# Kernel tuning notes

Measured on AMD Instinct MI355X. Metric: run time of the kernel, lower is better.

## Reference

```python
import jax, jax.numpy as jnp
import numpy as np

NEG_INF = -1.0e9
LN_EPS = 1e-5
LEAK = 0.2


def setup_inputs() -> dict:
    key = jax.random.key(0)
    ks = jax.random.split(key, 8)
    B, C, T, N, H = 8, 64, 24, 512, 2
    hd = C // H
    x = jax.random.normal(ks[0], (B, C, T, N), dtype=jnp.float32)
    gso = jax.random.randint(ks[1], (N, N), 0, 2, dtype=jnp.int32)
    # torch nn.Linear weights are (out, in); xavier-ish scale
    s = (2.0 / (C + C)) ** 0.5
    Wq = jax.random.normal(ks[2], (C, C), dtype=jnp.float32) * s
    Wk = jax.random.normal(ks[3], (C, C), dtype=jnp.float32) * s
    Wv = jax.random.normal(ks[4], (C, C), dtype=jnp.float32) * s
    sa = (2.0 / (H + hd)) ** 0.5
    a_src = jax.random.normal(ks[5], (H, hd), dtype=jnp.float32) * sa
    a_dst = jax.random.normal(ks[6], (H, hd), dtype=jnp.float32) * sa
    ln_gamma = jnp.ones((C,), dtype=jnp.float32)
    ln_beta = jnp.zeros((C,), dtype=jnp.float32)
    return {"x": x, "gso": gso, "Wq": Wq, "Wk": Wk, "Wv": Wv,
            "a_src": a_src, "a_dst": a_dst, "ln_gamma": ln_gamma, "ln_beta": ln_beta}


def _spatial_gat(x, gso, Wq, Wk, Wv, a_src, a_dst, ln_gamma, ln_beta):
    B, C, T, N = x.shape
    H, hd = a_src.shape
    # (B, C, T, N) -> (B*T, N, C)
    xr = jnp.transpose(x, (0, 2, 3, 1)).reshape(B * T, N, C)
    # torch Linear: y = x @ W.T
    Q = jnp.einsum('bnc,dc->bnd', xr, Wq).reshape(B * T, N, H, hd)
    K = jnp.einsum('bnc,dc->bnd', xr, Wk).reshape(B * T, N, H, hd)
    V = jnp.einsum('bnc,dc->bnd', xr, Wv).reshape(B * T, N, H, hd)
    # additive GAT scores, all heads at once
    s_src = jnp.einsum('bnhd,hd->bnh', Q, a_src)  # (BT, N, H)
    s_dst = jnp.einsum('bnhd,hd->bnh', K, a_dst)  # (BT, N, H)
    scores = jax.nn.leaky_relu(s_src[:, :, None, :] + s_dst[:, None, :, :], LEAK)  # (BT, Ni, Nj, H)
    mask = jnp.where(gso == 0, jnp.float32(NEG_INF), jnp.float32(0.0))  # (N, N)
    scores = scores + mask[None, :, :, None]
    attn = jax.nn.softmax(scores, axis=2)  # softmax over destination j
    out = jnp.einsum('bijh,bjhd->bihd', attn, V)  # (BT, N, H, hd)
    out = out.reshape(B * T, N, C)
    # LayerNorm over channel dim
    mu = jnp.mean(out, axis=-1, keepdims=True)
    var = jnp.var(out, axis=-1, keepdims=True)
    out = (out - mu) * jax.lax.rsqrt(var + LN_EPS) * ln_gamma + ln_beta
    # back to (B, C, T, N)
    return jnp.transpose(out.reshape(B, T, N, C), (0, 3, 1, 2))


def reference(x, gso, Wq, Wk, Wv, a_src, a_dst, ln_gamma, ln_beta):
    return _spatial_gat(x, gso, Wq, Wk, Wv, a_src, a_dst, ln_gamma, ln_beta)
```

## Files before the change

### kernel.cpp

```cpp
#include <hip/hip_runtime.h>

#define CDIM 64
#define TDIM 24
#define NDIM 512
#define NBT  192

typedef float    float4v __attribute__((ext_vector_type(4)));
typedef _Float16 half8v  __attribute__((ext_vector_type(8)));
typedef _Float16 half2v  __attribute__((ext_vector_type(2)));


__global__ void k0_maskbits(const int* __restrict__ gso, unsigned* __restrict__ bits) {
  int tg = blockIdx.x * 256 + threadIdx.x;
  int i  = tg >> 4;
  int ks = tg & 15;
  const int* row = gso + i * NDIM + ks * 32;
  unsigned w = 0;
#pragma unroll
  for (int b = 0; b < 32; ++b) w |= (row[b] != 0 ? (1u << b) : 0u);
  bits[ks * NDIM + i] = w;
}

struct SmemK1 {
  union {
    _Float16 xt[256][72];
    _Float16 vt[64][264];
  } big;
  _Float16 wv[64][72];
  _Float16 wext[16][72];
};

__launch_bounds__(256, 2)
__global__ void k1_qkv(const float* __restrict__ x,  const float* __restrict__ Wq,
                       const float* __restrict__ Wk, const float* __restrict__ Wv,
                       const float* __restrict__ a_src, const float* __restrict__ a_dst,
                       _Float16* __restrict__ VT_g,
                       float* __restrict__ s_src_g, float* __restrict__ s_dst_g) {
  __shared__ SmemK1 sm;
  const int t    = threadIdx.x;
  const int half = blockIdx.x;
  const int bt   = blockIdx.y;
  const int b    = bt / TDIM, tt = bt % TDIM;
  const int n0   = half * 256;

  for (int it = 0; it < 16; ++it) {
    int idx = it * 256 + t;
    int d = idx >> 6, k = idx & 63;
    sm.wv[d][k] = (_Float16)Wv[idx];
  }
  for (int it = 0; it < 32; ++it) {
    int idx = it * 256 + t;
    int cp  = idx >> 8;
    int n   = idx & 255;
    int c0  = cp * 2;
    const float* base = x + ((size_t)(b * CDIM + c0) * TDIM + tt) * NDIM + n0 + n;
    float v0 = base[0];
    float v1 = base[(size_t)TDIM * NDIM];
    half2v p; p[0] = (_Float16)v0; p[1] = (_Float16)v1;
    *(half2v*)&sm.big.xt[n][c0] = p;
  }
  for (int z = 4 * 72 + t; z < 16 * 72; z += 256) ((_Float16*)sm.wext)[z] = (_Float16)0.0f;
  if (t < 64) {
    int c = t;
    float s0 = 0.f, s1 = 0.f, d0 = 0.f, d1 = 0.f;
    for (int d = 0; d < 32; ++d) {
      s0 += a_src[d]      * Wq[d * 64 + c];
      s1 += a_src[32 + d] * Wq[(32 + d) * 64 + c];
      d0 += a_dst[d]      * Wk[d * 64 + c];
      d1 += a_dst[32 + d] * Wk[(32 + d) * 64 + c];
    }
    sm.wext[0][c] = (_Float16)s0; sm.wext[1][c] = (_Float16)s1;
    sm.wext[2][c] = (_Float16)d0; sm.wext[3][c] = (_Float16)d1;
  }
  __syncthreads();

  const int lane = t & 63, w = t >> 6;
  const int m = lane & 15, quad = lane >> 4;
  const int mbase = w * 64;

  float4v acc[4][5];
#pragma unroll
  for (int mt = 0; mt < 4; ++mt)
#pragma unroll
    for (int nt = 0; nt < 5; ++nt)
#pragma unroll
      for (int r = 0; r < 4; ++r) acc[mt][nt][r] = 0.f;

#pragma unroll
  for (int ks = 0; ks < 2; ++ks) {
    half8v af[4], bf[5];
#pragma unroll
    for (int mt = 0; mt < 4; ++mt)
      af[mt] = *(const half8v*)&sm.big.xt[mbase + mt * 16 + m][ks * 32 + quad * 8];
#pragma unroll
    for (int nt = 0; nt < 4; ++nt)
      bf[nt] = *(const half8v*)&sm.wv[nt * 16 + m][ks * 32 + quad * 8];
    bf[4] = *(const half8v*)&sm.wext[m][ks * 32 + quad * 8];
#pragma unroll
    for (int mt = 0; mt < 4; ++mt)
#pragma unroll
      for (int nt = 0; nt < 5; ++nt)
        acc[mt][nt] = __builtin_amdgcn_mfma_f32_16x16x32_f16(af[mt], bf[nt], acc[mt][nt], 0, 0, 0);
  }

  if (m < 4) {
    float* base = (m < 2 ? s_src_g : s_dst_g) + (size_t)(bt * 2 + (m & 1)) * NDIM;
#pragma unroll
    for (int mt = 0; mt < 4; ++mt)
#pragma unroll
      for (int r = 0; r < 4; ++r)
        base[n0 + mbase + mt * 16 + quad * 4 + r] = acc[mt][4][r];
  }
  __syncthreads();

#pragma unroll
  for (int mt = 0; mt < 4; ++mt)
#pragma unroll
    for (int nt = 0; nt < 4; ++nt)
#pragma unroll
      for (int r = 0; r < 4; ++r) {
        int node = mbase + mt * 16 + quad * 4 + r;
        int c    = nt * 16 + m;
        sm.big.vt[c][node] = (_Float16)acc[mt][nt][r];
      }
  __syncthreads();

  const unsigned* vts = (const unsigned*)sm.big.vt;
  unsigned* outdw = (unsigned*)VT_g;
  for (int it = 0; it < 32; ++it) {
    int idx = it * 256 + t;
    int c = idx >> 7, jd = idx & 127;
    outdw[(size_t)(bt * 64 + c) * 256 + half * 128 + jd] = vts[c * 132 + jd];
  }
}

struct SmemK2 {
  union {
    _Float16 vt[64][256];
    float otile[64][65];
  } big;
  union {
    float sdst[2][512];
    struct { float rsum[4][64]; float rsq[4][64]; float mu[64]; float rs[64]; } ln;
  } u2;
  float ssrc[2][64];
  unsigned maskT[16][64];
};

__launch_bounds__(256, 3)
__global__ void k2_attn(const _Float16* __restrict__ VT_g,
                        const float* __restrict__ s_src_g, const float* __restrict__ s_dst_g,
                        const unsigned* __restrict__ bits,
                        const float* __restrict__ gamma, const float* __restrict__ beta,
                        float* __restrict__ out) {
  __shared__ SmemK2 sm;
  const int t     = threadIdx.x;
  const int itile = blockIdx.x;
  const int bt    = blockIdx.y;
  const int i0    = itile * 64;
  const int b     = bt / TDIM, tt = bt % TDIM;

  for (int it = 0; it < 4; ++it) {
    int idx = it * 256 + t;
    ((float*)sm.u2.sdst)[idx] = s_dst_g[(size_t)bt * 2 * NDIM + idx];
  }
  if (t < 128) {
    int h = t >> 6, i = t & 63;
    sm.ssrc[h][i] = s_src_g[(size_t)(bt * 2 + h) * NDIM + i0 + i];
  }
  for (int it = 0; it < 4; ++it) {
    int idx = it * 256 + t;
    int ks = idx >> 6, i = idx & 63;
    sm.maskT[ks][i] = bits[ks * NDIM + i0 + i];
  }

  const int lane = t & 63, w = t >> 6;
  const int h = w >> 1, ihalf = w & 1;
  const int m = lane & 15, quad = lane >> 4;

  float4v acc[2][2];
#pragma unroll
  for (int mt = 0; mt < 2; ++mt)
#pragma unroll
    for (int nt = 0; nt < 2; ++nt)
#pragma unroll
      for (int r = 0; r < 4; ++r) acc[mt][nt][r] = 0.f;
  float ssum[2] = {0.f, 0.f};

  __syncthreads();
  float ss[2];
  ss[0] = sm.ssrc[h][ihalf * 32 + m];
  ss[1] = sm.ssrc[h][ihalf * 32 + 16 + m];

  for (int jh = 0; jh < 2; ++jh) {
    if (jh) __syncthreads();
    const unsigned* src_dw = (const unsigned*)VT_g + (size_t)bt * 64 * 256 + jh * 128;
    unsigned* vdw = (unsigned*)sm.big.vt;
    for (int it = 0; it < 32; ++it) {
      int idx = it * 256 + t;
      int c = idx >> 7, jd = idx & 127;
      vdw[c * 128 + (jd ^ ((c & 7) * 4))] = src_dw[(size_t)c * 256 + jd];
    }
    __syncthreads();

#pragma unroll
    for (int ksl = 0; ksl < 8; ++ksl) {
      int ks = jh * 8 + ksl;
      const float* dj = &sm.u2.sdst[h][ks * 32 + quad * 8];
      float djv[8];
#pragma unroll
      for (int q = 0; q < 8; ++q) djv[q] = dj[q];

      half8v af[2];
#pragma unroll
      for (int mt = 0; mt < 2; ++mt) {
        unsigned word = sm.maskT[ks][ihalf * 32 + mt * 16 + m];
        unsigned byte = (word >> (quad * 8)) & 0xffu;
        float s = ss[mt];
        half8v a;
        float lsum = 0.f;
#pragma unroll
        for (int jj = 0; jj < 8; ++jj) {
          float xv = s + djv[jj];
          xv = fmaxf(xv, 0.2f * xv);
          float e = ((byte >> jj) & 1u) ? __expf(xv - 4.f) : 0.f;
          _Float16 e16 = (_Float16)e;
          a[jj] = e16;
          lsum += (float)e16;
        }
        ssum[mt] += lsum;
        af[mt] = a;
      }
      int jo = ksl * 32 + quad * 8;
      int c0 = h * 32 + m, c1 = h * 32 + 16 + m;
      half8v b0 = *(const half8v*)&sm.big.vt[c0][jo ^ ((c0 & 7) * 8)];
      half8v b1 = *(const half8v*)&sm.big.vt[c1][jo ^ ((c1 & 7) * 8)];
      acc[0][0] = __builtin_amdgcn_mfma_f32_16x16x32_f16(af[0], b0, acc[0][0], 0, 0, 0);
      acc[0][1] = __builtin_amdgcn_mfma_f32_16x16x32_f16(af[0], b1, acc[0][1], 0, 0, 0);
      acc[1][0] = __builtin_amdgcn_mfma_f32_16x16x32_f16(af[1], b0, acc[1][0], 0, 0, 0);
      acc[1][1] = __builtin_amdgcn_mfma_f32_16x16x32_f16(af[1], b1, acc[1][1], 0, 0, 0);
    }
  }

#pragma unroll
  for (int mt = 0; mt < 2; ++mt) {
    ssum[mt] += __shfl_xor(ssum[mt], 16);
    ssum[mt] += __shfl_xor(ssum[mt], 32);
  }
  float inv[2] = {1.f / ssum[0], 1.f / ssum[1]};

  __syncthreads();
#pragma unroll
  for (int mt = 0; mt < 2; ++mt)
#pragma unroll
    for (int r = 0; r < 4; ++r) {
      float sv = __shfl(inv[mt], quad * 4 + r);
      int i_loc = ihalf * 32 + mt * 16 + quad * 4 + r;
#pragma unroll
      for (int nt = 0; nt < 2; ++nt) {
        int c = h * 32 + nt * 16 + m;
        sm.big.otile[i_loc][c] = acc[mt][nt][r] * sv;
      }
    }
  __syncthreads();

  {
    int i = t & 63, cg = t >> 6;
    float s1 = 0.f, s2 = 0.f;
#pragma unroll
    for (int cc = 0; cc < 16; ++cc) {
      float v = sm.big.otile[i][cg * 16 + cc];
      s1 += v; s2 += v * v;
    }
    sm.u2.ln.rsum[cg][i] = s1;
    sm.u2.ln.rsq[cg][i]  = s2;
  }
  __syncthreads();
  if (t < 64) {
    int i = t;
    float s1 = 0.f, s2 = 0.f;
#pragma unroll
    for (int cg = 0; cg < 4; ++cg) { s1 += sm.u2.ln.rsum[cg][i]; s2 += sm.u2.ln.rsq[cg][i]; }
    float mu  = s1 * (1.f / 64.f);
    float var = s2 * (1.f / 64.f) - mu * mu;
    sm.u2.ln.mu[i] = mu;
    sm.u2.ln.rs[i] = rsqrtf(var + 1e-5f);
  }
  __syncthreads();
  {
    int i = t & 63, cg = t >> 6;
    float mu = sm.u2.ln.mu[i], rs = sm.u2.ln.rs[i];
    int n = i0 + i;
#pragma unroll
    for (int cc = 0; cc < 16; ++cc) {
      int c = cg * 16 + cc;
      float v = (sm.big.otile[i][c] - mu) * rs * gamma[c] + beta[c];
      out[((size_t)(b * CDIM + c) * TDIM + tt) * NDIM + n] = v;
    }
  }
}

extern "C" void kernel_launch(void* const* d_in, const int* in_sizes, int n_in,
                              void* d_out, int out_size, void* d_ws, size_t ws_size,
                              hipStream_t stream) {
  const float* x     = (const float*)d_in[0];
  const int*   gso   = (const int*)d_in[1];
  const float* Wq    = (const float*)d_in[2];
  const float* Wk    = (const float*)d_in[3];
  const float* Wv    = (const float*)d_in[4];
  const float* a_src = (const float*)d_in[5];
  const float* a_dst = (const float*)d_in[6];
  const float* gamma = (const float*)d_in[7];
  const float* beta  = (const float*)d_in[8];
  float* out = (float*)d_out;

  char* ws = (char*)d_ws;
  _Float16* VT_g   = (_Float16*)ws;
  float*    s_src  = (float*)(ws + 12582912);
  float*    s_dst  = (float*)(ws + 13369344);
  unsigned* bits   = (unsigned*)(ws + 14155776);

  k0_maskbits<<<32, 256, 0, stream>>>(gso, bits);
  k1_qkv<<<dim3(2, NBT), 256, 0, stream>>>(x, Wq, Wk, Wv, a_src, a_dst, VT_g, s_src, s_dst);
  k2_attn<<<dim3(8, NBT), 256, 0, stream>>>(VT_g, s_src, s_dst, bits, gamma, beta, out);
}
```

Before: 145.9 us.

## Restructure mask to byte mask, compute softmax denominator via MFMA, shrink tiles

Mask bits become a byte mask (0x00/0xFF per half lane). In the attention kernel the mask is applied with a perm-and-AND on packed fp16 instead of per-element branches. The row-sum of exponentials is now computed by an extra MFMA against a ones vector, which replaces the scalar accumulation and shuffles. Leaky-relu is folded into a max of two FMAs. The folded a_src/a_dst weight projection moves into the prep kernel, and the QKV kernel uses 128-node tiles for higher occupancy. V tiles are streamed in four chunks with vectorised 16-byte loads. The cost is an extra MFMA per tile and smaller tiles in k2, which means more barriers.

After: 130.4 us. 10.6% less time.

```diff
diff --git a/kernel.cpp b/kernel.cpp
--- a/kernel.cpp
+++ b/kernel.cpp
@@ -10,77 +10,77 @@
 typedef _Float16 half2v  __attribute__((ext_vector_type(2)));
 
 
-__global__ void k0_maskbits(const int* __restrict__ gso, unsigned* __restrict__ bits) {
-  int tg = blockIdx.x * 256 + threadIdx.x;
-  int i  = tg >> 4;
-  int ks = tg & 15;
-  const int* row = gso + i * NDIM + ks * 32;
-  unsigned w = 0;
-#pragma unroll
-  for (int b = 0; b < 32; ++b) w |= (row[b] != 0 ? (1u << b) : 0u);
-  bits[ks * NDIM + i] = w;
+__global__ void k0_prep(const int* __restrict__ gso,
+                        const float* __restrict__ Wq, const float* __restrict__ Wk,
+                        const float* __restrict__ a_src, const float* __restrict__ a_dst,
+                        unsigned* __restrict__ maskb, float* __restrict__ wfold) {
+  int t = threadIdx.x;
+  if (blockIdx.x < 256) {
+    int tg = blockIdx.x * 256 + t;
+    int4 g = ((const int4*)gso)[tg];
+    unsigned w = (g.x ? 0x000000FFu : 0u) | (g.y ? 0x0000FF00u : 0u) |
+                 (g.z ? 0x00FF0000u : 0u) | (g.w ? 0xFF000000u : 0u);
+    maskb[tg] = w;
+  } else {
+    int r = t >> 6, c = t & 63;
+    const float* av = (r & 2) ? a_dst : a_src;
+    const float* W  = (r & 2) ? Wk : Wq;
+    int off = (r & 1) * 32;
+    float s = 0.f;
+#pragma unroll
+    for (int d = 0; d < 32; ++d)
+      s += av[off + d] * W[(off + d) * 64 + c];
+    wfold[t] = s;
+  }
 }
 
 struct SmemK1 {
   union {
-    _Float16 xt[256][72];
-    _Float16 vt[64][264];
+    _Float16 xt[128][72];
+    _Float16 vtb[64][136];
   } big;
   _Float16 wv[64][72];
   _Float16 wext[16][72];
 };
 
-__launch_bounds__(256, 2)
-__global__ void k1_qkv(const float* __restrict__ x,  const float* __restrict__ Wq,
-                       const float* __restrict__ Wk, const float* __restrict__ Wv,
-                       const float* __restrict__ a_src, const float* __restrict__ a_dst,
-                       _Float16* __restrict__ VT_g,
-                       float* __restrict__ s_src_g, float* __restrict__ s_dst_g) {
+__launch_bounds__(256, 4)
+__global__ void k1_v(const float* __restrict__ x, const float* __restrict__ Wv,
+                     const float* __restrict__ wfold,
+                     _Float16* __restrict__ VT_g,
+                     float* __restrict__ s_src_g, float* __restrict__ s_dst_g) {
   __shared__ SmemK1 sm;
-  const int t    = threadIdx.x;
-  const int half = blockIdx.x;
-  const int bt   = blockIdx.y;
-  const int b    = bt / TDIM, tt = bt % TDIM;
-  const int n0   = half * 256;
+  const int t  = threadIdx.x;
+  const int qn = blockIdx.x;
+  const int bt = blockIdx.y;
+  const int b  = bt / TDIM, tt = bt % TDIM;
+  const int n0 = qn * 128;
 
   for (int it = 0; it < 16; ++it) {
     int idx = it * 256 + t;
-    int d = idx >> 6, k = idx & 63;
-    sm.wv[d][k] = (_Float16)Wv[idx];
-  }
-  for (int it = 0; it < 32; ++it) {
+    sm.wv[idx >> 6][idx & 63] = (_Float16)Wv[idx];
+  }
+  for (int z = t; z < 12 * 72; z += 256) ((_Float16*)sm.wext[4])[z] = (_Float16)0.f;
+  {
+    int r = t >> 6, c = t & 63;
+    sm.wext[r][c] = (_Float16)wfold[t];
+  }
+  for (int it = 0; it < 16; ++it) {
     int idx = it * 256 + t;
-    int cp  = idx >> 8;
-    int n   = idx & 255;
-    int c0  = cp * 2;
+    int cp = idx >> 7, n = idx & 127;
+    int c0 = cp * 2;
     const float* base = x + ((size_t)(b * CDIM + c0) * TDIM + tt) * NDIM + n0 + n;
-    float v0 = base[0];
-    float v1 = base[(size_t)TDIM * NDIM];
-    half2v p; p[0] = (_Float16)v0; p[1] = (_Float16)v1;
+    half2v p; p[0] = (_Float16)base[0]; p[1] = (_Float16)base[(size_t)TDIM * NDIM];
     *(half2v*)&sm.big.xt[n][c0] = p;
-  }
-  for (int z = 4 * 72 + t; z < 16 * 72; z += 256) ((_Float16*)sm.wext)[z] = (_Float16)0.0f;
-  if (t < 64) {
-    int c = t;
-    float s0 = 0.f, s1 = 0.f, d0 = 0.f, d1 = 0.f;
-    for (int d = 0; d < 32; ++d) {
-      s0 += a_src[d]      * Wq[d * 64 + c];
-      s1 += a_src[32 + d] * Wq[(32 + d) * 64 + c];
-      d0 += a_dst[d]      * Wk[d * 64 + c];
-      d1 += a_dst[32 + d] * Wk[(32 + d) * 64 + c];
-    }
-    sm.wext[0][c] = (_Float16)s0; sm.wext[1][c] = (_Float16)s1;
-    sm.wext[2][c] = (_Float16)d0; sm.wext[3][c] = (_Float16)d1;
   }
   __syncthreads();
 
   const int lane = t & 63, w = t >> 6;
   const int m = lane & 15, quad = lane >> 4;
-  const int mbase = w * 64;
-
-  float4v acc[4][5];
-#pragma unroll
-  for (int mt = 0; mt < 4; ++mt)
+  const int mbase = w * 32;
+
+  float4v acc[2][5];
+#pragma unroll
+  for (int mt = 0; mt < 2; ++mt)
 #pragma unroll
     for (int nt = 0; nt < 5; ++nt)
 #pragma unroll
@@ -88,69 +88,67 @@
 
 #pragma unroll
   for (int ks = 0; ks < 2; ++ks) {
-    half8v af[4], bf[5];
-#pragma unroll
-    for (int mt = 0; mt < 4; ++mt)
+    half8v af[2], bf[5];
+#pragma unroll
+    for (int mt = 0; mt < 2; ++mt)
       af[mt] = *(const half8v*)&sm.big.xt[mbase + mt * 16 + m][ks * 32 + quad * 8];
 #pragma unroll
     for (int nt = 0; nt < 4; ++nt)
       bf[nt] = *(const half8v*)&sm.wv[nt * 16 + m][ks * 32 + quad * 8];
     bf[4] = *(const half8v*)&sm.wext[m][ks * 32 + quad * 8];
 #pragma unroll
-    for (int mt = 0; mt < 4; ++mt)
+    for (int mt = 0; mt < 2; ++mt)
 #pragma unroll
       for (int nt = 0; nt < 5; ++nt)
         acc[mt][nt] = __builtin_amdgcn_mfma_f32_16x16x32_f16(af[mt], bf[nt], acc[mt][nt], 0, 0, 0);
   }
 
   if (m < 4) {
-    float* base = (m < 2 ? s_src_g : s_dst_g) + (size_t)(bt * 2 + (m & 1)) * NDIM;
-#pragma unroll
-    for (int mt = 0; mt < 4; ++mt)
+    float* basep = (m < 2 ? s_src_g : s_dst_g) + (size_t)(bt * 2 + (m & 1)) * NDIM;
+#pragma unroll
+    for (int mt = 0; mt < 2; ++mt)
 #pragma unroll
       for (int r = 0; r < 4; ++r)
-        base[n0 + mbase + mt * 16 + quad * 4 + r] = acc[mt][4][r];
-  }
-  __syncthreads();
-
-#pragma unroll
-  for (int mt = 0; mt < 4; ++mt)
+        basep[n0 + mbase + mt * 16 + quad * 4 + r] = acc[mt][4][r];
+  }
+  __syncthreads();
+
+#pragma unroll
+  for (int mt = 0; mt < 2; ++mt)
 #pragma unroll
     for (int nt = 0; nt < 4; ++nt)
 #pragma unroll
-      for (int r = 0; r < 4; ++r) {
-        int node = mbase + mt * 16 + quad * 4 + r;
-        int c    = nt * 16 + m;
-        sm.big.vt[c][node] = (_Float16)acc[mt][nt][r];
+      for (int r = 0; r < 4; r += 2) {
+        int nl = mbase + mt * 16 + quad * 4 + r;
+        int c  = nt * 16 + m;
+        half2v p = __builtin_bit_cast(half2v,
+            __builtin_amdgcn_cvt_pkrtz(acc[mt][nt][r], acc[mt][nt][r + 1]));
+        *(half2v*)&sm.big.vtb[c][nl] = p;
       }
   __syncthreads();
 
-  const unsigned* vts = (const unsigned*)sm.big.vt;
+  const unsigned* vdw = (const unsigned*)sm.big.vtb;
   unsigned* outdw = (unsigned*)VT_g;
-  for (int it = 0; it < 32; ++it) {
+  for (int it = 0; it < 16; ++it) {
     int idx = it * 256 + t;
-    int c = idx >> 7, jd = idx & 127;
-    outdw[(size_t)(bt * 64 + c) * 256 + half * 128 + jd] = vts[c * 132 + jd];
+    int c = idx >> 6, jd = idx & 63;
+    outdw[(size_t)(bt * 64 + c) * 256 + qn * 64 + jd] = vdw[c * 68 + jd];
   }
 }
 
 struct SmemK2 {
   union {
-    _Float16 vt[64][256];
-    float otile[64][65];
-  } big;
-  union {
-    float sdst[2][512];
-    struct { float rsum[4][64]; float rsq[4][64]; float mu[64]; float rs[64]; } ln;
-  } u2;
-  float ssrc[2][64];
-  unsigned maskT[16][64];
+    struct { _Float16 vt[64][128]; unsigned char mb[64][144]; } s;
+    struct { float otile[64][66]; float rsum[4][64]; float rsq[4][64];
+             float mu[64]; float rs[64]; } e;
+  } u;
+  float sdst[2][512];
 };
 
-__launch_bounds__(256, 3)
+__launch_bounds__(256, 4)
 __global__ void k2_attn(const _Float16* __restrict__ VT_g,
                         const float* __restrict__ s_src_g, const float* __restrict__ s_dst_g,
-                        const unsigned* __restrict__ bits,
+                        const unsigned char* __restrict__ maskb,
                         const float* __restrict__ gamma, const float* __restrict__ beta,
                         float* __restrict__ out) {
   __shared__ SmemK2 sm;
@@ -159,108 +157,99 @@
   const int bt    = blockIdx.y;
   const int i0    = itile * 64;
   const int b     = bt / TDIM, tt = bt % TDIM;
+  const int lane  = t & 63, w = t >> 6;
+  const int h = w >> 1, ihalf = w & 1;
+  const int m = lane & 15, quad = lane >> 4;
 
   for (int it = 0; it < 4; ++it) {
     int idx = it * 256 + t;
-    ((float*)sm.u2.sdst)[idx] = s_dst_g[(size_t)bt * 2 * NDIM + idx];
-  }
-  if (t < 128) {
-    int h = t >> 6, i = t & 63;
-    sm.ssrc[h][i] = s_src_g[(size_t)(bt * 2 + h) * NDIM + i0 + i];
-  }
-  for (int it = 0; it < 4; ++it) {
-    int idx = it * 256 + t;
-    int ks = idx >> 6, i = idx & 63;
-    sm.maskT[ks][i] = bits[ks * NDIM + i0 + i];
-  }
-
-  const int lane = t & 63, w = t >> 6;
-  const int h = w >> 1, ihalf = w & 1;
-  const int m = lane & 15, quad = lane >> 4;
-
-  float4v acc[2][2];
+    ((float*)sm.sdst)[idx] = s_dst_g[(size_t)bt * 2 * NDIM + idx];
+  }
+  float s1r[2], s2r[2];
+#pragma unroll
+  for (int mt = 0; mt < 2; ++mt) {
+    float sv = s_src_g[(size_t)(bt * 2 + h) * NDIM + i0 + ihalf * 32 + mt * 16 + m];
+    s1r[mt] = sv - 4.f;
+    s2r[mt] = 0.2f * sv - 4.f;
+  }
+
+  float4v acc[2][2], accs[2];
+#pragma unroll
+  for (int mt = 0; mt < 2; ++mt) {
+#pragma unroll
+    for (int r = 0; r < 4; ++r) { acc[mt][0][r] = 0.f; acc[mt][1][r] = 0.f; accs[mt][r] = 0.f; }
+  }
+  const half8v bones = {(_Float16)1.f, (_Float16)1.f, (_Float16)1.f, (_Float16)1.f,
+                        (_Float16)1.f, (_Float16)1.f, (_Float16)1.f, (_Float16)1.f};
+
+  for (int js = 0; js < 4; ++js) {
+    __syncthreads();
+    {
+      const uint4* vsrc = (const uint4*)VT_g;
+#pragma unroll
+      for (int it = 0; it < 4; ++it) {
+        int idx = it * 256 + t;
+        int c = idx >> 4, ch = idx & 15;
+        uint4 val = vsrc[(size_t)(bt * 64 + c) * 64 + js * 16 + ch];
+        *(uint4*)&sm.u.s.vt[c][(ch * 8) ^ ((c & 7) * 8)] = val;
+      }
+#pragma unroll
+      for (int it = 0; it < 2; ++it) {
+        int idx = it * 256 + t;
+        int c = idx >> 3, ch = idx & 7;
+        uint4 mv = *(const uint4*)(maskb + (size_t)(i0 + c) * NDIM + js * 128 + ch * 16);
+        *(uint4*)&sm.u.s.mb[c][ch * 16] = mv;
+      }
+    }
+    __syncthreads();
+
+#pragma unroll
+    for (int ksl = 0; ksl < 4; ++ksl) {
+      int jq = ksl * 32 + quad * 8;
+      float4v dj0 = *(const float4v*)&sm.sdst[h][js * 128 + jq];
+      float4v dj1 = *(const float4v*)&sm.sdst[h][js * 128 + jq + 4];
+      int vbase = (h * 32 + m) * 128 + (jq ^ ((m & 7) * 8));
+      half8v b0 = *(const half8v*)&sm.u.s.vt[0][vbase];
+      half8v b1 = *(const half8v*)&sm.u.s.vt[0][vbase + 16 * 128];
+#pragma unroll
+      for (int mt = 0; mt < 2; ++mt) {
+        const unsigned* mwp = (const unsigned*)&sm.u.s.mb[ihalf * 32 + mt * 16 + m][jq];
+        unsigned mw0 = mwp[0], mw1 = mwp[1];
+        float e[8];
+#pragma unroll
+        for (int jj = 0; jj < 8; ++jj) {
+          float d = (jj < 4) ? dj0[jj] : dj1[jj - 4];
+          float f1 = s1r[mt] + d;
+          float f2 = __builtin_fmaf(d, 0.2f, s2r[mt]);
+          e[jj] = __expf(fmaxf(f1, f2));
+        }
+        unsigned p0 = __builtin_bit_cast(unsigned, __builtin_amdgcn_cvt_pkrtz(e[0], e[1]))
+                      & __builtin_amdgcn_perm(0u, mw0, 0x01010000u);
+        unsigned p1 = __builtin_bit_cast(unsigned, __builtin_amdgcn_cvt_pkrtz(e[2], e[3]))
+                      & __builtin_amdgcn_perm(0u, mw0, 0x03030202u);
+        unsigned p2 = __builtin_bit_cast(unsigned, __builtin_amdgcn_cvt_pkrtz(e[4], e[5]))
+                      & __builtin_amdgcn_perm(0u, mw1, 0x01010000u);
+        unsigned p3 = __builtin_bit_cast(unsigned, __builtin_amdgcn_cvt_pkrtz(e[6], e[7]))
+                      & __builtin_amdgcn_perm(0u, mw1, 0x03030202u);
+        uint4 au; au.x = p0; au.y = p1; au.z = p2; au.w = p3;
+        half8v af = __builtin_bit_cast(half8v, au);
+        acc[mt][0] = __builtin_amdgcn_mfma_f32_16x16x32_f16(af, b0,    acc[mt][0], 0, 0, 0);
+        acc[mt][1] = __builtin_amdgcn_mfma_f32_16x16x32_f16(af, b1,    acc[mt][1], 0, 0, 0);
+        accs[mt]   = __builtin_amdgcn_mfma_f32_16x16x32_f16(af, bones, accs[mt],   0, 0, 0);
+      }
+    }
+  }
+
+  __syncthreads();
 #pragma unroll
   for (int mt = 0; mt < 2; ++mt)
 #pragma unroll
-    for (int nt = 0; nt < 2; ++nt)
-#pragma unroll
-      for (int r = 0; r < 4; ++r) acc[mt][nt][r] = 0.f;
-  float ssum[2] = {0.f, 0.f};
-
-  __syncthreads();
-  float ss[2];
-  ss[0] = sm.ssrc[h][ihalf * 32 + m];
-  ss[1] = sm.ssrc[h][ihalf * 32 + 16 + m];
-
-  for (int jh = 0; jh < 2; ++jh) {
-    if (jh) __syncthreads();
-    const unsigned* src_dw = (const unsigned*)VT_g + (size_t)bt * 64 * 256 + jh * 128;
-    unsigned* vdw = (unsigned*)sm.big.vt;
-    for (int it = 0; it < 32; ++it) {
-      int idx = it * 256 + t;
-      int c = idx >> 7, jd = idx & 127;
-      vdw[c * 128 + (jd ^ ((c & 7) * 4))] = src_dw[(size_t)c * 256 + jd];
-    }
-    __syncthreads();
-
-#pragma unroll
-    for (int ksl = 0; ksl < 8; ++ksl) {
-      int ks = jh * 8 + ksl;
-      const float* dj = &sm.u2.sdst[h][ks * 32 + quad * 8];
-      float djv[8];
-#pragma unroll
-      for (int q = 0; q < 8; ++q) djv[q] = dj[q];
-
-      half8v af[2];
-#pragma unroll
-      for (int mt = 0; mt < 2; ++mt) {
-        unsigned word = sm.maskT[ks][ihalf * 32 + mt * 16 + m];
-        unsigned byte = (word >> (quad * 8)) & 0xffu;
-        float s = ss[mt];
-        half8v a;
-        float lsum = 0.f;
-#pragma unroll
-        for (int jj = 0; jj < 8; ++jj) {
-          float xv = s + djv[jj];
-          xv = fmaxf(xv, 0.2f * xv);
-          float e = ((byte >> jj) & 1u) ? __expf(xv - 4.f) : 0.f;
-          _Float16 e16 = (_Float16)e;
-          a[jj] = e16;
-          lsum += (float)e16;
-        }
-        ssum[mt] += lsum;
-        af[mt] = a;
-      }
-      int jo = ksl * 32 + quad * 8;
-      int c0 = h * 32 + m, c1 = h * 32 + 16 + m;
-      half8v b0 = *(const half8v*)&sm.big.vt[c0][jo ^ ((c0 & 7) * 8)];
-      half8v b1 = *(const half8v*)&sm.big.vt[c1][jo ^ ((c1 & 7) * 8)];
-      acc[0][0] = __builtin_amdgcn_mfma_f32_16x16x32_f16(af[0], b0, acc[0][0], 0, 0, 0);
-      acc[0][1] = __builtin_amdgcn_mfma_f32_16x16x32_f16(af[0], b1, acc[0][1], 0, 0, 0);
-      acc[1][0] = __builtin_amdgcn_mfma_f32_16x16x32_f16(af[1], b0, acc[1][0], 0, 0, 0);
-      acc[1][1] = __builtin_amdgcn_mfma_f32_16x16x32_f16(af[1], b1, acc[1][1], 0, 0, 0);
-    }
-  }
-
-#pragma unroll
-  for (int mt = 0; mt < 2; ++mt) {
-    ssum[mt] += __shfl_xor(ssum[mt], 16);
-    ssum[mt] += __shfl_xor(ssum[mt], 32);
-  }
-  float inv[2] = {1.f / ssum[0], 1.f / ssum[1]};
-
-  __syncthreads();
-#pragma unroll
-  for (int mt = 0; mt < 2; ++mt)
-#pragma unroll
     for (int r = 0; r < 4; ++r) {
-      float sv = __shfl(inv[mt], quad * 4 + r);
+      float sc = __builtin_amdgcn_rcpf(accs[mt][r]);
       int i_loc = ihalf * 32 + mt * 16 + quad * 4 + r;
 #pragma unroll
-      for (int nt = 0; nt < 2; ++nt) {
-        int c = h * 32 + nt * 16 + m;
-        sm.big.otile[i_loc][c] = acc[mt][nt][r] * sv;
-      }
+      for (int nt = 0; nt < 2; ++nt)
+        sm.u.e.otile[i_loc][h * 32 + nt * 16 + m] = acc[mt][nt][r] * sc;
     }
   __syncthreads();
 
@@ -269,32 +258,32 @@
     float s1 = 0.f, s2 = 0.f;
 #pragma unroll
     for (int cc = 0; cc < 16; ++cc) {
-      float v = sm.big.otile[i][cg * 16 + cc];
+      float v = sm.u.e.otile[i][cg * 16 + cc];
       s1 += v; s2 += v * v;
     }
-    sm.u2.ln.rsum[cg][i] = s1;
-    sm.u2.ln.rsq[cg][i]  = s2;
+    sm.u.e.rsum[cg][i] = s1;
+    sm.u.e.rsq[cg][i]  = s2;
   }
   __syncthreads();
   if (t < 64) {
     int i = t;
     float s1 = 0.f, s2 = 0.f;
 #pragma unroll
-    for (int cg = 0; cg < 4; ++cg) { s1 += sm.u2.ln.rsum[cg][i]; s2 += sm.u2.ln.rsq[cg][i]; }
+    for (int cg = 0; cg < 4; ++cg) { s1 += sm.u.e.rsum[cg][i]; s2 += sm.u.e.rsq[cg][i]; }
     float mu  = s1 * (1.f / 64.f);
     float var = s2 * (1.f / 64.f) - mu * mu;
-    sm.u2.ln.mu[i] = mu;
-    sm.u2.ln.rs[i] = rsqrtf(var + 1e-5f);
+    sm.u.e.mu[i] = mu;
+    sm.u.e.rs[i] = rsqrtf(var + 1e-5f);
   }
   __syncthreads();
   {
     int i = t & 63, cg = t >> 6;
-    float mu = sm.u2.ln.mu[i], rs = sm.u2.ln.rs[i];
+    float mu = sm.u.e.mu[i], rs = sm.u.e.rs[i];
     int n = i0 + i;
 #pragma unroll
     for (int cc = 0; cc < 16; ++cc) {
       int c = cg * 16 + cc;
-      float v = (sm.big.otile[i][c] - mu) * rs * gamma[c] + beta[c];
+      float v = (sm.u.e.otile[i][c] - mu) * rs * gamma[c] + beta[c];
       out[((size_t)(b * CDIM + c) * TDIM + tt) * NDIM + n] = v;
     }
   }
@@ -315,12 +304,13 @@
   float* out = (float*)d_out;
 
   char* ws = (char*)d_ws;
-  _Float16* VT_g   = (_Float16*)ws;
-  float*    s_src  = (float*)(ws + 12582912);
-  float*    s_dst  = (float*)(ws + 13369344);
-  unsigned* bits   = (unsigned*)(ws + 14155776);
-
-  k0_maskbits<<<32, 256, 0, stream>>>(gso, bits);
-  k1_qkv<<<dim3(2, NBT), 256, 0, stream>>>(x, Wq, Wk, Wv, a_src, a_dst, VT_g, s_src, s_dst);
-  k2_attn<<<dim3(8, NBT), 256, 0, stream>>>(VT_g, s_src, s_dst, bits, gamma, beta, out);
+  _Float16* VT_g  = (_Float16*)ws;
+  float*    s_src = (float*)(ws + 12582912);
+  float*    s_dst = (float*)(ws + 13369344);
+  unsigned char* maskb = (unsigned char*)(ws + 14155776);
+  float*    wfold = (float*)(ws + 14417920);
+
+  k0_prep<<<257, 256, 0, stream>>>(gso, Wq, Wk, a_src, a_dst, (unsigned*)maskb, wfold);
+  k1_v<<<dim3(4, NBT), 256, 0, stream>>>(x, Wv, wfold, VT_g, s_src, s_dst);
+  k2_attn<<<dim3(8, NBT), 256, 0, stream>>>(VT_g, s_src, s_dst, maskb, gamma, beta, out);
 }
```
